# Performance work log

Hardware: AMD Instinct MI355X
Metric: run time of the kernel (lower is better)

## Reference

```python
import jax, jax.numpy as jnp
import numpy as np
from jax import lax

WBITS = 4
BN_EPS = 1e-5


def quantize_weight_symmetric(w, wbits=WBITS):
    # Per-tensor symmetric uniform quantization with straight-through estimator.
    qmax = float(2 ** (wbits - 1) - 1)  # 7 for 4-bit
    scale = jnp.max(jnp.abs(w)) / qmax
    wq = jnp.clip(jnp.round(w / scale), -qmax, qmax) * scale
    # STE: forward uses wq, backward passes gradient straight through to w
    return w + lax.stop_gradient(wq - w)


def setup_inputs() -> dict:
    key = jax.random.key(0)
    k1, k2 = jax.random.split(key)
    x = jax.random.normal(k1, (32, 128, 56, 56), dtype=jnp.float32)
    w = jax.random.normal(k2, (256, 128, 3, 3), dtype=jnp.float32) * 0.05
    gamma = jnp.ones((256,), dtype=jnp.float32)
    beta = jnp.zeros((256,), dtype=jnp.float32)
    return {"x": x, "w": w, "gamma": gamma, "beta": beta}


def reference(x, w, gamma, beta):
    # Quantized conv (QConv, bias=False, stride=1, padding=1)
    wq = quantize_weight_symmetric(w)
    out = lax.conv_general_dilated(
        x, wq,
        window_strides=(1, 1),
        padding=[(1, 1), (1, 1)],
        dimension_numbers=("NCHW", "OIHW", "NCHW"),
    )  # [N, 256, 56, 56]
    # BatchNorm2d in training mode: batch statistics over (N, H, W)
    mean = jnp.mean(out, axis=(0, 2, 3))
    var = jnp.var(out, axis=(0, 2, 3))
    inv = gamma * lax.rsqrt(var + BN_EPS)
    out = out * inv[None, :, None, None] + (beta - mean * inv)[None, :, None, None]
    # abits=32 -> full-precision activation (ReLU)
    return jax.nn.relu(out)
```

## Files before the change

### kernel.cpp

```cpp
#include <hip/hip_runtime.h>

typedef unsigned short u16;
typedef unsigned int u32;
typedef __attribute__((ext_vector_type(4))) float f32x4;
typedef __attribute__((ext_vector_type(8))) short short8;

#define HWD 56
#define HW2 3136
#define C_IN 128
#define K_OUT 256
#define N_IMG 32
#define CHW_IN 401408
#define PIX 100352
#define WQ_N 294912
#define XP 58
#define XPP 3364
#define XT_PER_N (XPP*128)
#define NSLICE 1568
#define CV_OFF 33554432u
#define WS_NEED_BF16 (CV_OFF + (size_t)PIX * K_OUT * 2)

__device__ __forceinline__ u16 f2bf(float f) {
    u32 u = __float_as_uint(f);
    u32 r = u + 0x7FFFu + ((u >> 16) & 1u);
    return (u16)(r >> 16);
}

__device__ __forceinline__ void glds16(const u16* g, u16* l) {
    __builtin_amdgcn_global_load_lds(
        (const __attribute__((address_space(1))) void*)g,
        (__attribute__((address_space(3))) void*)l, 16, 0, 0);
}

__global__ void maxabs_k(const float* __restrict__ w, u32* __restrict__ wsmax) {
    float m = 0.f;
    for (int i = blockIdx.x * blockDim.x + threadIdx.x; i < WQ_N; i += gridDim.x * blockDim.x)
        m = fmaxf(m, fabsf(w[i]));
    for (int off = 32; off; off >>= 1)
        m = fmaxf(m, __shfl_xor(m, off));
    __shared__ float sm[4];
    int lane = threadIdx.x & 63, wid = threadIdx.x >> 6;
    if (lane == 0) sm[wid] = m;
    __syncthreads();
    if (threadIdx.x == 0) {
        float mm = fmaxf(fmaxf(sm[0], sm[1]), fmaxf(sm[2], sm[3]));
        atomicMax(wsmax, __float_as_uint(mm));
    }
}

__global__ void quant_t_k3(const float* __restrict__ w, const u32* __restrict__ wsmax,
                           u16* __restrict__ wqt3) {
    int o = blockIdx.x * 256 + threadIdx.x;
    if (o >= WQ_N) return;
    int j = o & 7;
    int r1 = o >> 3;
    int mrow = r1 & 127;
    int r2 = r1 >> 7;
    int oct = r2 & 3;
    int r3 = r2 >> 2;
    int mt = r3 & 1;
    int kt = r3 >> 1;
    int m = mt * 128 + mrow;
    int tap = kt >> 2, cq = kt & 3;
    int c = cq * 32 + oct * 8 + j;
    float scale = __uint_as_float(wsmax[0]) / 7.0f;
    float q = rintf(w[(m * 128 + c) * 9 + tap] / scale);
    q = fminf(fmaxf(q, -7.0f), 7.0f);
    wqt3[o] = f2bf(q * scale);
}

__global__ void halo_zero(u16* __restrict__ xt) {
    int i = blockIdx.x * 256 + threadIdx.x;
    if (i >= 32 * 3648) return;
    int n = i / 3648, t = i - n * 3648;
    int site = t >> 4, chunk = t & 15;
    int h, w;
    if (site < 58)       { h = 0;          w = site; }
    else if (site < 116) { h = 57;         w = site - 58; }
    else if (site < 172) { h = site - 115; w = 0; }
    else                 { h = site - 171; w = 57; }
    *(uint4*)(xt + ((size_t)n * XPP + h * XP + w) * 128 + chunk * 8) = (uint4){0, 0, 0, 0};
}

__global__ __launch_bounds__(256) void pad_transpose(const float* __restrict__ x,
                                                     u16* __restrict__ xt) {
    __shared__ float T[128][57];
    const int tid = threadIdx.x;
    const int n = blockIdx.x / HWD;
    const int h = blockIdx.x - n * HWD;
    const float* src = x + (size_t)n * CHW_IN + h * HWD;
    #pragma unroll
    for (int it = 0; it < 7; ++it) {
        int i = tid + it * 256;
        int c = i / 14, q = i - c * 14;
        float4 v = *(const float4*)(src + c * HW2 + q * 4);
        T[c][q * 4 + 0] = v.x; T[c][q * 4 + 1] = v.y;
        T[c][q * 4 + 2] = v.z; T[c][q * 4 + 3] = v.w;
    }
    __syncthreads();
    u16* dst = xt + ((size_t)n * XPP + (h + 1) * XP + 1) * 128;
    #pragma unroll
    for (int it = 0; it < 4; ++it) {
        int i = tid + it * 256;
        if (i < 56 * 16) {
            int w = i >> 4, oc = i & 15;
            union { u16 us[8]; uint4 v4; } pk;
            #pragma unroll
            for (int j = 0; j < 8; ++j) pk.us[j] = f2bf(T[oc * 8 + j][w]);
            *(uint4*)(dst + (size_t)w * 128 + oc * 8) = pk.v4;
        }
    }
}

template <bool BF16OUT>
__global__ __launch_bounds__(256, 3) void conv_m(const u16* __restrict__ xt,
                                                 const u16* __restrict__ wqt3,
                                                 float* __restrict__ out,
                                                 u16* __restrict__ cvout,
                                                 float* __restrict__ P) {
    __shared__ __align__(16) u16 lds[3][2][4096];
    const int tid = threadIdx.x;
    const int lane = tid & 63;
    const int w4 = tid >> 6;
    const int wm = w4 >> 1, wn = w4 & 1;
    const int fr = lane & 15, fq = lane >> 4;
    const int swz = (blockIdx.x & 7) * 196 + (blockIdx.x >> 3);
    const int nt = swz >> 1, mt = swz & 1;
    const int pixbase = nt * 128;

    u32 siteE[2];
    #pragma unroll
    for (int i = 0; i < 2; ++i) {
        int p = pixbase + i * 64 + lane;
        int n = p / HW2; int hw = p - n * HW2;
        int h = hw / HWD; int ww = hw - h * HWD;
        siteE[i] = (u32)(n * XT_PER_N + (h * XP + ww) * 128);
    }

#define STAGE(AB, BB, kt_) do {                                                   \
        const int tap_ = (kt_) >> 2, cq_ = (kt_) & 3;                             \
        const int r_ = tap_ / 3, s_ = tap_ - r_ * 3;                              \
        const u16* ga_ = wqt3 + ((kt_) * 2 + mt) * 4096 + (w4 * 2) * 512 + lane * 8; \
        glds16(ga_,       (AB) + (w4 * 2 + 0) * 512);                             \
        glds16(ga_ + 512, (AB) + (w4 * 2 + 1) * 512);                             \
        const u32 be_ = (u32)((r_ * XP + s_) * 128 + cq_ * 32 + w4 * 8);          \
        glds16(xt + siteE[0] + be_, (BB) + w4 * 1024 + 0);                        \
        glds16(xt + siteE[1] + be_, (BB) + w4 * 1024 + 512);                      \
    } while (0)
#define PHASE_BODY(Acur, Bcur) do {                                               \
        short8 af[4], bf[4];                                                      \
        _Pragma("unroll") for (int mi = 0; mi < 4; ++mi)                          \
            af[mi] = *(const short8*)&(Acur)[fq * 1024 + (wm * 64 + mi * 16 + fr) * 8]; \
        _Pragma("unroll") for (int ni = 0; ni < 4; ++ni)                          \
            bf[ni] = *(const short8*)&(Bcur)[fq * 1024 + (wn * 64 + ni * 16 + fr) * 8]; \
        asm volatile("s_waitcnt lgkmcnt(0)" ::: "memory");                        \
        __builtin_amdgcn_sched_barrier(0);                                        \
        __builtin_amdgcn_s_setprio(1);                                            \
        _Pragma("unroll") for (int mi = 0; mi < 4; ++mi)                          \
            _Pragma("unroll") for (int ni = 0; ni < 4; ++ni)                      \
                acc[mi][ni] = __builtin_amdgcn_mfma_f32_16x16x32_bf16(            \
                    af[mi], bf[ni], acc[mi][ni], 0, 0, 0);                        \
        __builtin_amdgcn_s_setprio(0);                                            \
    } while (0)
#define BAR() __builtin_amdgcn_s_barrier()
#define GATE(n_) asm volatile("s_waitcnt vmcnt(" #n_ ")" ::: "memory")

    f32x4 acc[4][4];
    #pragma unroll
    for (int a = 0; a < 4; ++a)
        #pragma unroll
        for (int b = 0; b < 4; ++b)
            acc[a][b] = (f32x4){0.f, 0.f, 0.f, 0.f};

    STAGE(&lds[0][0][0], &lds[0][1][0], 0);
    STAGE(&lds[1][0][0], &lds[1][1][0], 1);
    GATE(4);
    BAR();

    #pragma unroll 1
    for (int tt = 0; tt < 12; ++tt) {
        #pragma unroll
        for (int u = 0; u < 3; ++u) {
            const int t = tt * 3 + u;
            const int bs = (u + 2) % 3;
            if (t < 34) STAGE(&lds[bs][0][0], &lds[bs][1][0], t + 2);
            PHASE_BODY(&lds[u][0][0], &lds[u][1][0]);
            if (t < 34) GATE(4);
            else if (t == 34) GATE(0);
            BAR();
        }
    }
#undef STAGE
#undef PHASE_BODY
#undef GATE

    const int slice = nt * 2 + wn;
    #pragma unroll
    for (int mi = 0; mi < 4; ++mi)
        #pragma unroll
        for (int j = 0; j < 4; ++j) {
            float s = 0.f, q = 0.f;
            #pragma unroll
            for (int ni = 0; ni < 4; ++ni) {
                float v = acc[mi][ni][j];
                s += v; q += v * v;
            }
            #pragma unroll
            for (int msk = 1; msk < 16; msk <<= 1) {
                s += __shfl_xor(s, msk);
                q += __shfl_xor(q, msk);
            }
            if (fr == 0) {
                int ch = mt * 128 + wm * 64 + mi * 16 + fq * 4 + j;
                float* dst = P + ((size_t)ch * NSLICE + slice) * 2;
                dst[0] = s; dst[1] = q;
            }
        }

    if (BF16OUT) {
        u16* T = (u16*)&lds[0][0][0];
        #pragma unroll
        for (int mi = 0; mi < 4; ++mi)
            #pragma unroll
            for (int ni = 0; ni < 4; ++ni) {
                int px_l = wn * 64 + ni * 16 + fr;
                int ch_l = wm * 64 + mi * 16 + fq * 4;
                #pragma unroll
                for (int j = 0; j < 4; ++j)
                    T[(ch_l + j) * 136 + px_l] = f2bf(acc[mi][ni][j]);
            }
        __syncthreads();
        #pragma unroll
        for (int it = 0; it < 8; ++it) {
            int q = tid + it * 256;
            int ch_l = q >> 4, pg = q & 15;
            uint4 v = *(const uint4*)&T[ch_l * 136 + pg * 8];
            *(uint4*)&cvout[(size_t)(mt * 128 + ch_l) * PIX + pixbase + pg * 8] = v;
        }
    } else {
        #pragma unroll
        for (int ni = 0; ni < 4; ++ni) {
            int pix = pixbase + wn * 64 + ni * 16 + fr;
            int n = pix / HW2;
            int hw = pix - n * HW2;
            size_t obase = (size_t)n * (K_OUT * HW2) + hw;
            #pragma unroll
            for (int mi = 0; mi < 4; ++mi) {
                int ch = mt * 128 + wm * 64 + mi * 16 + fq * 4;
                #pragma unroll
                for (int j = 0; j < 4; ++j)
                    out[obase + (size_t)(ch + j) * HW2] = acc[mi][ni][j];
            }
        }
    }
#undef BAR
}

__global__ void stats_fin(const float* __restrict__ P, const float* __restrict__ gamma,
                          const float* __restrict__ beta, float* __restrict__ stats) {
    int ch = blockIdx.x;
    int tid = threadIdx.x;
    float s = 0.f, q = 0.f;
    const float* base = P + (size_t)ch * NSLICE * 2;
    for (int i = tid; i < NSLICE; i += 256) {
        float2 v = *(const float2*)(base + i * 2);
        s += v.x; q += v.y;
    }
    for (int m = 32; m; m >>= 1) { s += __shfl_xor(s, m); q += __shfl_xor(q, m); }
    __shared__ float ss[4], qs[4];
    int l = tid & 63, w = tid >> 6;
    if (l == 0) { ss[w] = s; qs[w] = q; }
    __syncthreads();
    if (tid == 0) {
        float S = ss[0] + ss[1] + ss[2] + ss[3];
        float Q = qs[0] + qs[1] + qs[2] + qs[3];
        float mean = S / (float)PIX;
        float var = Q / (float)PIX - mean * mean;
        float inv = gamma[ch] * rsqrtf(var + 1e-5f);
        stats[2 * ch] = inv;
        stats[2 * ch + 1] = beta[ch] - mean * inv;
    }
}

__global__ void bn_relu_nchw(const u16* __restrict__ cvout, float* __restrict__ out,
                             const float* __restrict__ stats) {
    const int b = blockIdx.x;
    const int ch = b / 49, g = b - ch * 49;
    const float inv = stats[2 * ch], sh = stats[2 * ch + 1];
    const int p8 = (g * 256 + threadIdx.x) * 8;
    short8 v = *(const short8*)&cvout[(size_t)ch * PIX + p8];
    const int n = p8 / HW2;
    const int hw = p8 - n * HW2;
    float* dst = out + ((size_t)n * K_OUT + ch) * HW2 + hw;
    f32x4 o0, o1;
    #pragma unroll
    for (int j = 0; j < 4; ++j) {
        float a = __uint_as_float(((u32)(u16)v[j]) << 16);
        float bb = __uint_as_float(((u32)(u16)v[j + 4]) << 16);
        o0[j] = fmaxf(a * inv + sh, 0.f);
        o1[j] = fmaxf(bb * inv + sh, 0.f);
    }
    *(f32x4*)dst = o0;
    *(f32x4*)(dst + 4) = o1;
}

__global__ void bn_relu_f32(float* __restrict__ out, const float* __restrict__ stats) {
    const int n4 = ((size_t)N_IMG * K_OUT * HW2) / 4;
    int stride = gridDim.x * blockDim.x;
    for (int i = blockIdx.x * blockDim.x + threadIdx.x; i < n4; i += stride) {
        int ch = (i / (HW2 / 4)) & (K_OUT - 1);
        float inv = stats[2 * ch], sh = stats[2 * ch + 1];
        f32x4 v = ((f32x4*)out)[i];
        #pragma unroll
        for (int j = 0; j < 4; ++j)
            v[j] = fmaxf(v[j] * inv + sh, 0.f);
        ((f32x4*)out)[i] = v;
    }
}

extern "C" void kernel_launch(void* const* d_in, const int* in_sizes, int n_in,
                              void* d_out, int out_size, void* d_ws, size_t ws_size,
                              hipStream_t stream) {
    const float* x = (const float*)d_in[0];
    const float* w = (const float*)d_in[1];
    const float* gamma = (const float*)d_in[2];
    const float* beta = (const float*)d_in[3];
    float* out = (float*)d_out;

    char* ws = (char*)d_ws;
    u32* wsmax = (u32*)ws;
    float* stats = (float*)(ws + 64);
    u16* wqt3 = (u16*)(ws + 4096);
    u16* xt = (u16*)(ws + (1u << 20));
    float* P = (float*)(ws + 29360128u);
    u16* cvout = (u16*)(ws + CV_OFF);
    const bool bf16path = (ws_size >= WS_NEED_BF16);

    hipMemsetAsync(wsmax, 0, 64, stream);
    maxabs_k<<<128, 256, 0, stream>>>(w, wsmax);
    quant_t_k3<<<WQ_N / 256, 256, 0, stream>>>(w, wsmax, wqt3);
    halo_zero<<<456, 256, 0, stream>>>(xt);
    pad_transpose<<<N_IMG * HWD, 256, 0, stream>>>(x, xt);
    if (bf16path) {
        conv_m<true><<<1568, 256, 0, stream>>>(xt, wqt3, out, cvout, P);
        stats_fin<<<K_OUT, 256, 0, stream>>>(P, gamma, beta, stats);
        bn_relu_nchw<<<K_OUT * 49, 256, 0, stream>>>(cvout, out, stats);
    } else {
        conv_m<false><<<1568, 256, 0, stream>>>(xt, wqt3, out, cvout, P);
        stats_fin<<<K_OUT, 256, 0, stream>>>(P, gamma, beta, stats);
        bn_relu_f32<<<4096, 256, 0, stream>>>(out, stats);
    }
}
```

Before: 147.0 us.

## Re-layout padded input by channel-quarter rows and loop both M tiles per block

The padded bf16 input now uses a layout where each image row is split into four 32-channel quarter rows, so each staged B tile reads contiguous 32-channel pixel runs. The B fragment LDS indexing changes to match. Each conv block now handles both 128-channel output tiles in sequence, halving the grid so the input tile is reused from cache across the two M passes. The explicit lgkmcnt wait inside the phase is dropped in favour of sched barriers, which shifts scheduling onto the compiler. The halved grid gives fewer blocks to spread across the CUs, and the two passes run serially inside each block.

Measured after the change: 155.3 us. +5.7%, slower.

```diff
diff --git a/kernel.cpp b/kernel.cpp
--- a/kernel.cpp
+++ b/kernel.cpp
@@ -13,9 +13,9 @@
 #define CHW_IN 401408
 #define PIX 100352
 #define WQ_N 294912
-#define XP 58
-#define XPP 3364
-#define XT_PER_N (XPP*128)
+#define X2_ROW 1856
+#define X2_H 7424
+#define X2_N 430592
 #define NSLICE 1568
 #define CV_OFF 33554432u
 #define WS_NEED_BF16 (CV_OFF + (size_t)PIX * K_OUT * 2)
@@ -69,51 +69,55 @@
     wqt3[o] = f2bf(q * scale);
 }
 
-__global__ void halo_zero(u16* __restrict__ xt) {
+__global__ void halo_zero(u16* __restrict__ xt2) {
     int i = blockIdx.x * 256 + threadIdx.x;
     if (i >= 32 * 3648) return;
     int n = i / 3648, t = i - n * 3648;
-    int site = t >> 4, chunk = t & 15;
+    int site = t >> 4, c16 = t & 15;
     int h, w;
     if (site < 58)       { h = 0;          w = site; }
     else if (site < 116) { h = 57;         w = site - 58; }
     else if (site < 172) { h = site - 115; w = 0; }
     else                 { h = site - 171; w = 57; }
-    *(uint4*)(xt + ((size_t)n * XPP + h * XP + w) * 128 + chunk * 8) = (uint4){0, 0, 0, 0};
+    int cq = c16 >> 2, o4 = c16 & 3;
+    *(uint4*)(xt2 + (size_t)n * X2_N + h * X2_H + cq * X2_ROW + w * 32 + o4 * 8) =
+        (uint4){0, 0, 0, 0};
 }
 
 __global__ __launch_bounds__(256) void pad_transpose(const float* __restrict__ x,
-                                                     u16* __restrict__ xt) {
+                                                     u16* __restrict__ xt2) {
     __shared__ float T[128][57];
     const int tid = threadIdx.x;
     const int n = blockIdx.x / HWD;
     const int h = blockIdx.x - n * HWD;
-    const float* src = x + (size_t)n * CHW_IN + h * HWD;
+    const float* src = x + (size_t)n * CHW_IN + h * HW2;
+    const float* srow = x + (size_t)n * CHW_IN + h * HWD;
     #pragma unroll
     for (int it = 0; it < 7; ++it) {
         int i = tid + it * 256;
         int c = i / 14, q = i - c * 14;
-        float4 v = *(const float4*)(src + c * HW2 + q * 4);
+        float4 v = *(const float4*)(srow + c * HW2 + q * 4);
         T[c][q * 4 + 0] = v.x; T[c][q * 4 + 1] = v.y;
         T[c][q * 4 + 2] = v.z; T[c][q * 4 + 3] = v.w;
     }
     __syncthreads();
-    u16* dst = xt + ((size_t)n * XPP + (h + 1) * XP + 1) * 128;
+    u16* drow = xt2 + (size_t)n * X2_N + (h + 1) * X2_H;
     #pragma unroll
     for (int it = 0; it < 4; ++it) {
         int i = tid + it * 256;
         if (i < 56 * 16) {
             int w = i >> 4, oc = i & 15;
+            int cq = oc >> 2, o4 = oc & 3;
             union { u16 us[8]; uint4 v4; } pk;
             #pragma unroll
             for (int j = 0; j < 8; ++j) pk.us[j] = f2bf(T[oc * 8 + j][w]);
-            *(uint4*)(dst + (size_t)w * 128 + oc * 8) = pk.v4;
+            *(uint4*)(drow + cq * X2_ROW + (w + 1) * 32 + o4 * 8) = pk.v4;
         }
     }
 }
 
 template <bool BF16OUT>
-__global__ __launch_bounds__(256, 3) void conv_m(const u16* __restrict__ xt,
+__global__ __launch_bounds__(256, 3) void conv_m(const u16* __restrict__ xt2,
                                                  const u16* __restrict__ wqt3,
                                                  float* __restrict__ out,
                                                  u16* __restrict__ cvout,
@@ -124,37 +128,34 @@
     const int w4 = tid >> 6;
     const int wm = w4 >> 1, wn = w4 & 1;
     const int fr = lane & 15, fq = lane >> 4;
-    const int swz = (blockIdx.x & 7) * 196 + (blockIdx.x >> 3);
-    const int nt = swz >> 1, mt = swz & 1;
+    const int nt = (blockIdx.x & 7) * 98 + (blockIdx.x >> 3);
     const int pixbase = nt * 128;
 
-    u32 siteE[2];
+    u32 siteL[2];
     #pragma unroll
-    for (int i = 0; i < 2; ++i) {
-        int p = pixbase + i * 64 + lane;
+    for (int j = 0; j < 2; ++j) {
+        int p = pixbase + w4 * 32 + j * 16 + (lane >> 2);
         int n = p / HW2; int hw = p - n * HW2;
         int h = hw / HWD; int ww = hw - h * HWD;
-        siteE[i] = (u32)(n * XT_PER_N + (h * XP + ww) * 128);
-    }
-
-#define STAGE(AB, BB, kt_) do {                                                   \
+        siteL[j] = (u32)(n * X2_N + h * X2_H + ww * 32 + (lane & 3) * 8);
+    }
+
+#define STAGE(AB, BB, kt_, mt_) do {                                              \
         const int tap_ = (kt_) >> 2, cq_ = (kt_) & 3;                             \
         const int r_ = tap_ / 3, s_ = tap_ - r_ * 3;                              \
-        const u16* ga_ = wqt3 + ((kt_) * 2 + mt) * 4096 + (w4 * 2) * 512 + lane * 8; \
+        const u16* ga_ = wqt3 + ((kt_) * 2 + (mt_)) * 4096 + (w4 * 2) * 512 + lane * 8; \
         glds16(ga_,       (AB) + (w4 * 2 + 0) * 512);                             \
         glds16(ga_ + 512, (AB) + (w4 * 2 + 1) * 512);                             \
-        const u32 be_ = (u32)((r_ * XP + s_) * 128 + cq_ * 32 + w4 * 8);          \
-        glds16(xt + siteE[0] + be_, (BB) + w4 * 1024 + 0);                        \
-        glds16(xt + siteE[1] + be_, (BB) + w4 * 1024 + 512);                      \
+        const u32 D_ = (u32)((r_ * 4 + cq_) * X2_ROW + s_ * 32);                  \
+        glds16(xt2 + siteL[0] + D_, (BB) + w4 * 1024 + 0);                        \
+        glds16(xt2 + siteL[1] + D_, (BB) + w4 * 1024 + 512);                      \
     } while (0)
 #define PHASE_BODY(Acur, Bcur) do {                                               \
         short8 af[4], bf[4];                                                      \
         _Pragma("unroll") for (int mi = 0; mi < 4; ++mi)                          \
             af[mi] = *(const short8*)&(Acur)[fq * 1024 + (wm * 64 + mi * 16 + fr) * 8]; \
         _Pragma("unroll") for (int ni = 0; ni < 4; ++ni)                          \
-            bf[ni] = *(const short8*)&(Bcur)[fq * 1024 + (wn * 64 + ni * 16 + fr) * 8]; \
-        asm volatile("s_waitcnt lgkmcnt(0)" ::: "memory");                        \
-        __builtin_amdgcn_sched_barrier(0);                                        \
+            bf[ni] = *(const short8*)&(Bcur)[(wn * 64 + ni * 16 + fr) * 32 + fq * 8]; \
         __builtin_amdgcn_s_setprio(1);                                            \
         _Pragma("unroll") for (int mi = 0; mi < 4; ++mi)                          \
             _Pragma("unroll") for (int ni = 0; ni < 4; ++ni)                      \
@@ -163,97 +164,107 @@
         __builtin_amdgcn_s_setprio(0);                                            \
     } while (0)
 #define BAR() __builtin_amdgcn_s_barrier()
+#define SCHED0() __builtin_amdgcn_sched_barrier(0)
 #define GATE(n_) asm volatile("s_waitcnt vmcnt(" #n_ ")" ::: "memory")
 
     f32x4 acc[4][4];
-    #pragma unroll
-    for (int a = 0; a < 4; ++a)
+
+    #pragma unroll 1
+    for (int mt = 0; mt < 2; ++mt) {
         #pragma unroll
-        for (int b = 0; b < 4; ++b)
-            acc[a][b] = (f32x4){0.f, 0.f, 0.f, 0.f};
-
-    STAGE(&lds[0][0][0], &lds[0][1][0], 0);
-    STAGE(&lds[1][0][0], &lds[1][1][0], 1);
-    GATE(4);
-    BAR();
-
-    #pragma unroll 1
-    for (int tt = 0; tt < 12; ++tt) {
+        for (int a = 0; a < 4; ++a)
+            #pragma unroll
+            for (int b = 0; b < 4; ++b)
+                acc[a][b] = (f32x4){0.f, 0.f, 0.f, 0.f};
+
+        STAGE(&lds[0][0][0], &lds[0][1][0], 0, mt);
+        STAGE(&lds[1][0][0], &lds[1][1][0], 1, mt);
+        GATE(4);
+        BAR();
+
+        #pragma unroll 1
+        for (int tt = 0; tt < 12; ++tt) {
+            #pragma unroll
+            for (int u = 0; u < 3; ++u) {
+                const int t = tt * 3 + u;
+                const int bs = (u + 2) % 3;
+                SCHED0();
+                if (t < 34) STAGE(&lds[bs][0][0], &lds[bs][1][0], t + 2, mt);
+                PHASE_BODY(&lds[u][0][0], &lds[u][1][0]);
+                SCHED0();
+                if (t < 34) GATE(4);
+                else if (t == 34) GATE(0);
+                BAR();
+            }
+        }
+
+        const int slice = nt * 2 + wn;
         #pragma unroll
-        for (int u = 0; u < 3; ++u) {
-            const int t = tt * 3 + u;
-            const int bs = (u + 2) % 3;
-            if (t < 34) STAGE(&lds[bs][0][0], &lds[bs][1][0], t + 2);
-            PHASE_BODY(&lds[u][0][0], &lds[u][1][0]);
-            if (t < 34) GATE(4);
-            else if (t == 34) GATE(0);
-            BAR();
+        for (int mi = 0; mi < 4; ++mi)
+            #pragma unroll
+            for (int j = 0; j < 4; ++j) {
+                float s = 0.f, q = 0.f;
+                #pragma unroll
+                for (int ni = 0; ni < 4; ++ni) {
+                    float v = acc[mi][ni][j];
+                    s += v; q += v * v;
+                }
+                #pragma unroll
+                for (int msk = 1; msk < 16; msk <<= 1) {
+                    s += __shfl_xor(s, msk);
+                    q += __shfl_xor(q, msk);
+                }
+                if (fr == 0) {
+                    int ch = mt * 128 + wm * 64 + mi * 16 + fq * 4 + j;
+                    float* dst = P + ((size_t)ch * NSLICE + slice) * 2;
+                    dst[0] = s; dst[1] = q;
+                }
+            }
+
+        if (BF16OUT) {
+            u16* T = (u16*)&lds[0][0][0];
+            #pragma unroll
+            for (int mi = 0; mi < 4; ++mi)
+                #pragma unroll
+                for (int ni = 0; ni < 4; ++ni) {
+                    int px_l = wn * 64 + ni * 16 + fr;
+                    int ch_l = wm * 64 + mi * 16 + fq * 4;
+                    #pragma unroll
+                    for (int j = 0; j < 4; ++j)
+                        T[(ch_l + j) * 136 + px_l] = f2bf(acc[mi][ni][j]);
+                }
+            __syncthreads();
+            #pragma unroll
+            for (int it = 0; it < 8; ++it) {
+                int q = tid + it * 256;
+                int ch_l = q >> 4, pg = q & 15;
+                uint4 v = *(const uint4*)&T[ch_l * 136 + pg * 8];
+                *(uint4*)&cvout[(size_t)(mt * 128 + ch_l) * PIX + pixbase + pg * 8] = v;
+            }
+            __syncthreads();
+        } else {
+            #pragma unroll
+            for (int ni = 0; ni < 4; ++ni) {
+                int pix = pixbase + wn * 64 + ni * 16 + fr;
+                int n = pix / HW2;
+                int hw = pix - n * HW2;
+                size_t obase = (size_t)n * (K_OUT * HW2) + hw;
+                #pragma unroll
+                for (int mi = 0; mi < 4; ++mi) {
+                    int ch = mt * 128 + wm * 64 + mi * 16 + fq * 4;
+                    #pragma unroll
+                    for (int j = 0; j < 4; ++j)
+                        out[obase + (size_t)(ch + j) * HW2] = acc[mi][ni][j];
+                }
+            }
+            __syncthreads();
         }
     }
 #undef STAGE
 #undef PHASE_BODY
+#undef BAR
+#undef SCHED0
 #undef GATE
-
-    const int slice = nt * 2 + wn;
-    #pragma unroll
-    for (int mi = 0; mi < 4; ++mi)
-        #pragma unroll
-        for (int j = 0; j < 4; ++j) {
-            float s = 0.f, q = 0.f;
-            #pragma unroll
-            for (int ni = 0; ni < 4; ++ni) {
-                float v = acc[mi][ni][j];
-                s += v; q += v * v;
-            }
-            #pragma unroll
-            for (int msk = 1; msk < 16; msk <<= 1) {
-                s += __shfl_xor(s, msk);
-                q += __shfl_xor(q, msk);
-            }
-            if (fr == 0) {
-                int ch = mt * 128 + wm * 64 + mi * 16 + fq * 4 + j;
-                float* dst = P + ((size_t)ch * NSLICE + slice) * 2;
-                dst[0] = s; dst[1] = q;
-            }
-        }
-
-    if (BF16OUT) {
-        u16* T = (u16*)&lds[0][0][0];
-        #pragma unroll
-        for (int mi = 0; mi < 4; ++mi)
-            #pragma unroll
-            for (int ni = 0; ni < 4; ++ni) {
-                int px_l = wn * 64 + ni * 16 + fr;
-                int ch_l = wm * 64 + mi * 16 + fq * 4;
-                #pragma unroll
-                for (int j = 0; j < 4; ++j)
-                    T[(ch_l + j) * 136 + px_l] = f2bf(acc[mi][ni][j]);
-            }
-        __syncthreads();
-        #pragma unroll
-        for (int it = 0; it < 8; ++it) {
-            int q = tid + it * 256;
-            int ch_l = q >> 4, pg = q & 15;
-            uint4 v = *(const uint4*)&T[ch_l * 136 + pg * 8];
-            *(uint4*)&cvout[(size_t)(mt * 128 + ch_l) * PIX + pixbase + pg * 8] = v;
-        }
-    } else {
-        #pragma unroll
-        for (int ni = 0; ni < 4; ++ni) {
-            int pix = pixbase + wn * 64 + ni * 16 + fr;
-            int n = pix / HW2;
-            int hw = pix - n * HW2;
-            size_t obase = (size_t)n * (K_OUT * HW2) + hw;
-            #pragma unroll
-            for (int mi = 0; mi < 4; ++mi) {
-                int ch = mt * 128 + wm * 64 + mi * 16 + fq * 4;
-                #pragma unroll
-                for (int j = 0; j < 4; ++j)
-                    out[obase + (size_t)(ch + j) * HW2] = acc[mi][ni][j];
-            }
-        }
-    }
-#undef BAR
 }
 
 __global__ void stats_fin(const float* __restrict__ P, const float* __restrict__ gamma,
@@ -331,7 +342,7 @@
     u32* wsmax = (u32*)ws;
     float* stats = (float*)(ws + 64);
     u16* wqt3 = (u16*)(ws + 4096);
-    u16* xt = (u16*)(ws + (1u << 20));
+    u16* xt2 = (u16*)(ws + (1u << 20));
     float* P = (float*)(ws + 29360128u);
     u16* cvout = (u16*)(ws + CV_OFF);
     const bool bf16path = (ws_size >= WS_NEED_BF16);
@@ -339,14 +350,14 @@
     hipMemsetAsync(wsmax, 0, 64, stream);
     maxabs_k<<<128, 256, 0, stream>>>(w, wsmax);
     quant_t_k3<<<WQ_N / 256, 256, 0, stream>>>(w, wsmax, wqt3);
-    halo_zero<<<456, 256, 0, stream>>>(xt);
-    pad_transpose<<<N_IMG * HWD, 256, 0, stream>>>(x, xt);
+    halo_zero<<<456, 256, 0, stream>>>(xt2);
+    pad_transpose<<<N_IMG * HWD, 256, 0, stream>>>(x, xt2);
     if (bf16path) {
-        conv_m<true><<<1568, 256, 0, stream>>>(xt, wqt3, out, cvout, P);
+        conv_m<true><<<784, 256, 0, stream>>>(xt2, wqt3, out, cvout, P);
         stats_fin<<<K_OUT, 256, 0, stream>>>(P, gamma, beta, stats);
         bn_relu_nchw<<<K_OUT * 49, 256, 0, stream>>>(cvout, out, stats);
     } else {
-        conv_m<false><<<1568, 256, 0, stream>>>(xt, wqt3, out, cvout, P);
+        conv_m<false><<<784, 256, 0, stream>>>(xt2, wqt3, out, cvout, P);
         stats_fin<<<K_OUT, 256, 0, stream>>>(P, gamma, beta, stats);
         bn_relu_f32<<<4096, 256, 0, stream>>>(out, stats);
     }
```
